# Kernel tuning notes

Measured on AMD Instinct MI355X. Metric: run time of the kernel, lower is better.

The kernel has to match this reference:

```python
import jax, jax.numpy as jnp
import numpy as np

LN_EPS = 1e-5
SCALE = 1.0 / 8.0  # 1/sqrt(dim/num_heads) = 1/sqrt(64)


def layernorm(x, g, b):
    m = jnp.mean(x, axis=-1, keepdims=True)
    v = jnp.mean(jnp.square(x - m), axis=-1, keepdims=True)
    return (x - m) * jax.lax.rsqrt(v + LN_EPS) * g + b


def attention_block(q_in, kv_in, wq, bq, wk, bk, wv, bv, g, b):
    # un-split single-matrix attention, faithful to the source (no head reshape)
    Q = q_in @ wq + bq            # [B,S,D]
    K = kv_in @ wk + bk           # [B,T,D]
    V = kv_in @ wv + bv           # [B,T,D]
    scores = jnp.einsum('bsd,btd->bst', Q, K) * SCALE  # [B,S,T]
    A = jax.nn.softmax(scores, axis=-1)
    out = jnp.einsum('bst,btd->bsd', A, V)
    return layernorm(out + q_in, g, b)


def setup_inputs() -> dict:
    key = jax.random.key(0)
    ks = jax.random.split(key, 16)
    B, S, T, D = 4, 2048, 2048, 1024
    w = lambda k: jax.random.normal(k, (D, D), dtype=jnp.float32) * 0.02
    z = jnp.zeros((D,), dtype=jnp.float32)
    o = jnp.ones((D,), dtype=jnp.float32)
    return {
        'x': jax.random.normal(ks[0], (B, S, D), dtype=jnp.float32),
        'y': jax.random.normal(ks[1], (B, T, D), dtype=jnp.float32),
        'wq_m': w(ks[2]), 'bq_m': z, 'wk_m': w(ks[3]), 'bk_m': z,
        'wv_m': w(ks[4]), 'bv_m': z, 'g_m': o, 'b_m': z,
        'wq_c': w(ks[5]), 'bq_c': z, 'wk_c': w(ks[6]), 'bk_c': z,
        'wv_c': w(ks[7]), 'bv_c': z, 'g_c': o, 'b_c': z,
        'f0_w': w(ks[8]), 'f0_b': z, 'f1_w': w(ks[9]), 'f1_b': z,
        'g_d': o, 'b_d': z,
    }


def reference(x, y,
              wq_m, bq_m, wk_m, bk_m, wv_m, bv_m, g_m, b_m,
              wq_c, bq_c, wk_c, bk_c, wv_c, bv_c, g_c, b_c,
              f0_w, f0_b, f1_w, f1_b, g_d, b_d):
    # masked (self) attention + shared decoder LN residual
    res = x
    x = layernorm(attention_block(x, x, wq_m, bq_m, wk_m, bk_m, wv_m, bv_m, g_m, b_m) + res, g_d, b_d)
    # cross attention against memory y
    res = x
    x = layernorm(attention_block(x, y, wq_c, bq_c, wk_c, bk_c, wv_c, bv_c, g_c, b_c) + res, g_d, b_d)
    # FFN: loop condition in source is always true -> GELU (exact) after every layer
    res = x
    x = jax.nn.gelu(x @ f0_w + f0_b, approximate=False)
    x = jax.nn.gelu(x @ f1_w + f1_b, approximate=False)
    return layernorm(x + res, g_d, b_d)
```

## Files before the change

kernel.cpp:

```cpp
#include <hip/hip_runtime.h>

#define DEV __device__ __forceinline__

typedef __attribute__((ext_vector_type(8))) short bf16x8;
typedef __attribute__((ext_vector_type(4))) float f32x4;

DEV float bf2f(unsigned short u) { return __uint_as_float(((unsigned int)u) << 16); }
DEV unsigned short f2bf(float f) {
    unsigned int x = __float_as_uint(f);
    return (unsigned short)((x + 0x7fffu + ((x >> 16) & 1u)) >> 16);
}
DEV float gelu_exact(float x) { return 0.5f * x * (1.0f + erff(x * 0.7071067811865475f)); }

DEV void gload16(const void* g, void* l) {
    __builtin_amdgcn_global_load_lds((const __attribute__((address_space(1))) void*)g,
                                     (__attribute__((address_space(3))) void*)l, 16, 0, 0);
}

template <int OFF>
DEV bf16x8 ds_read128(unsigned addr) {
    bf16x8 r;
    asm volatile("ds_read_b128 %0, %1 offset:%2" : "=v"(r) : "v"(addr), "i"(OFF));
    return r;
}

__global__ __launch_bounds__(256) void transpose_cast_w(const float* __restrict__ in,
                                                        unsigned short* __restrict__ out,
                                                        int R, int C) {
    __shared__ float tile[32][33];
    int c0 = blockIdx.x * 32, r0 = blockIdx.y * 32;
    int tx = threadIdx.x, ty = threadIdx.y;
#pragma unroll
    for (int i = 0; i < 32; i += 8)
        tile[ty + i][tx] = in[(size_t)(r0 + ty + i) * C + (c0 + tx)];
    __syncthreads();
#pragma unroll
    for (int i = 0; i < 32; i += 8)
        out[(size_t)(c0 + ty + i) * R + (r0 + tx)] = f2bf(tile[tx][ty + i]);
}

__global__ __launch_bounds__(256) void cast_f32_bf16(const float* __restrict__ in,
                                                     unsigned short* __restrict__ out, int n4) {
    int i = blockIdx.x * 256 + threadIdx.x;
    if (i >= n4) return;
    float4 v = ((const float4*)in)[i];
    unsigned short o[4] = {f2bf(v.x), f2bf(v.y), f2bf(v.z), f2bf(v.w)};
    *(uint2*)(out + (size_t)i * 4) = *(uint2*)o;
}


template <int H>
DEV void mfma16q(const bf16x8 (&a)[2][2], const bf16x8 (&b)[4][2], f32x4 (&acc)[4][4]) {
#pragma unroll
    for (int ks = 0; ks < 2; ++ks)
#pragma unroll
        for (int n = 0; n < 4; ++n) {
            acc[2 * H][n]     = __builtin_amdgcn_mfma_f32_16x16x32_bf16(a[0][ks], b[n][ks], acc[2 * H][n], 0, 0, 0);
            acc[2 * H + 1][n] = __builtin_amdgcn_mfma_f32_16x16x32_bf16(a[1][ks], b[n][ks], acc[2 * H + 1][n], 0, 0, 0);
        }
}

template <int BIAS_MODE, bool GELU_ACT, bool OUT_F32>
__global__ __launch_bounds__(256, 2) void gemm128(const unsigned short* __restrict__ A,
                                                  const unsigned short* __restrict__ BT,
                                                  const float* __restrict__ bias,
                                                  float* __restrict__ Cf,
                                                  unsigned short* __restrict__ Cb,
                                                  int N, int K, int lda, int ldb, float scale,
                                                  long sA, long sB, long sC, long sBias) {
    const int gx = gridDim.x, gy = gridDim.y;
    int f = blockIdx.x + gx * (blockIdx.y + gy * blockIdx.z);
    const int nwg = gx * gy * gridDim.z;
    f = (f & 7) * (nwg >> 3) + (f >> 3);
    const int bz = f / (gx * gy);
    const int rem = f - bz * gx * gy;
    const int by = rem / gx;
    const int bx = rem - by * gx;

    A += (long)bz * sA;
    BT += (long)bz * sB;
    if (BIAS_MODE) bias += (long)bz * sBias;

    const int tid = threadIdx.x;
    const int lane = tid & 63;
    const int wave = tid >> 6;
    const int wr = wave >> 1;
    const int wc = wave & 1;
    const int llo = lane & 15, lhi = lane >> 4;
    const int bm = bx * 128, bn = by * 128;

    __shared__ unsigned short lds[2][2][128 * 64];

    const int xk0 = (0 + lhi) ^ (llo & 7);
    const int xk1 = (4 + lhi) ^ (llo & 7);

    const unsigned base0 = (unsigned)(size_t)&lds[0][0][0];
    const unsigned aA0 = base0 + (unsigned)(wr * 64 + llo) * 128u + xk0 * 16;
    const unsigned aA1 = base0 + (unsigned)(wr * 64 + llo) * 128u + xk1 * 16;
    const unsigned aB0 = base0 + (unsigned)(wc * 64 + llo) * 128u + xk0 * 16;
    const unsigned aB1 = base0 + (unsigned)(wc * 64 + llo) * 128u + xk1 * 16;

    int srow[4], sq[4];
#pragma unroll
    for (int L = 0; L < 4; ++L) {
        const int d = L * 256 + tid;
        srow[L] = d >> 3;
        sq[L] = (d & 7) ^ (srow[L] & 7);
    }
    const unsigned short* gA = A + (size_t)bm * lda;
    const unsigned short* gB = BT + (size_t)bn * ldb;

#define SA(kt, BUF)                                                                     \
    {                                                                                   \
        _Pragma("unroll") for (int L = 0; L < 4; ++L)                                   \
            gload16(gA + (size_t)srow[L] * lda + (kt) + sq[L] * 8,                      \
                    &lds[BUF][0][(L * 256 + wave * 64) * 8]);                           \
    }
#define SB(kt, BUF)                                                                     \
    {                                                                                   \
        _Pragma("unroll") for (int L = 0; L < 4; ++L)                                   \
            gload16(gB + (size_t)srow[L] * ldb + (kt) + sq[L] * 8,                      \
                    &lds[BUF][1][(L * 256 + wave * 64) * 8]);                           \
    }

    f32x4 acc[4][4] = {};
    bf16x8 b[4][2];

#define PH(H, BUF, LOADB, STG, TAIL)                                         \
    {                                                                        \
        STG;                                                                 \
        bf16x8 afr[2][2];                                                    \
        afr[0][0] = ds_read128<(BUF)*32768 + (H)*4096 + 0>(aA0);             \
        afr[0][1] = ds_read128<(BUF)*32768 + (H)*4096 + 0>(aA1);             \
        afr[1][0] = ds_read128<(BUF)*32768 + (H)*4096 + 2048>(aA0);          \
        afr[1][1] = ds_read128<(BUF)*32768 + (H)*4096 + 2048>(aA1);          \
        if (LOADB) {                                                         \
            b[0][0] = ds_read128<(BUF)*32768 + 16384 + 0>(aB0);              \
            b[0][1] = ds_read128<(BUF)*32768 + 16384 + 0>(aB1);              \
            b[1][0] = ds_read128<(BUF)*32768 + 16384 + 2048>(aB0);           \
            b[1][1] = ds_read128<(BUF)*32768 + 16384 + 2048>(aB1);           \
            b[2][0] = ds_read128<(BUF)*32768 + 16384 + 4096>(aB0);           \
            b[2][1] = ds_read128<(BUF)*32768 + 16384 + 4096>(aB1);           \
            b[3][0] = ds_read128<(BUF)*32768 + 16384 + 6144>(aB0);           \
            b[3][1] = ds_read128<(BUF)*32768 + 16384 + 6144>(aB1);           \
        }                                                                    \
        __builtin_amdgcn_s_barrier();                                        \
        asm volatile("s_waitcnt lgkmcnt(0)" :::);                            \
        __builtin_amdgcn_sched_barrier(0);                                   \
        __builtin_amdgcn_s_setprio(1);                                       \
        mfma16q<H>(afr, b, acc);                                             \
        __builtin_amdgcn_s_setprio(0);                                       \
        TAIL;                                                                \
        __builtin_amdgcn_s_barrier();                                        \
    }

#define VM0 asm volatile("s_waitcnt vmcnt(0)" :::)
#define NOP ((void)0)

    const int nt = K >> 6;

    SA(0, 0);
    SB(0, 0);
    VM0;
    __builtin_amdgcn_s_barrier();

    int kt = 0;
    for (int t = 0; t < nt; t += 2) {
        const bool st0 = (t + 1 < nt);
        const bool st1 = (t + 2 < nt);
        PH(0, 0, true,  if (st0) { SA(kt + 64, 1); SB(kt + 64, 1); }, NOP);
        PH(1, 0, false, NOP, VM0);
        PH(0, 1, true,  if (st1) { SA(kt + 128, 0); SB(kt + 128, 0); }, NOP);
        PH(1, 1, false, NOP, VM0);
        kt += 128;
    }
#undef PH
#undef SA
#undef SB
#undef VM0
#undef NOP

#pragma unroll
    for (int m = 0; m < 4; ++m) {
#pragma unroll
        for (int n = 0; n < 4; ++n) {
            const int col = bn + wc * 64 + n * 16 + llo;
            float bcol = 0.f;
            if constexpr (BIAS_MODE == 1) bcol = bias[col];
#pragma unroll
            for (int j = 0; j < 4; ++j) {
                const int row = bm + wr * 64 + m * 16 + lhi * 4 + j;
                float v = acc[m][n][j] * scale + bcol;
                if constexpr (BIAS_MODE == 2) v += bias[row];
                if constexpr (GELU_ACT) v = gelu_exact(v);
                const size_t idx = (size_t)bz * (size_t)sC + (size_t)row * N + col;
                if constexpr (OUT_F32) Cf[idx] = v;
                else Cb[idx] = f2bf(v);
            }
        }
    }
}

__global__ __launch_bounds__(256) void softmax_rows(unsigned short* __restrict__ s, int T) {
    __shared__ float red[4];
    unsigned short* p = s + (size_t)blockIdx.x * T;
    const int tid = threadIdx.x;

    uint4 raw = *(const uint4*)(p + tid * 8);
    const unsigned short* u = (const unsigned short*)&raw;
    float v[8];
#pragma unroll
    for (int j = 0; j < 8; ++j) v[j] = bf2f(u[j]);

    float mx = -3.4e38f;
#pragma unroll
    for (int j = 0; j < 8; ++j) mx = fmaxf(mx, v[j]);
#pragma unroll
    for (int o = 32; o; o >>= 1) mx = fmaxf(mx, __shfl_xor(mx, o));
    if ((tid & 63) == 0) red[tid >> 6] = mx;
    __syncthreads();
    mx = fmaxf(fmaxf(red[0], red[1]), fmaxf(red[2], red[3]));
    __syncthreads();

    float sum = 0.f;
#pragma unroll
    for (int j = 0; j < 8; ++j) {
        v[j] = expf(v[j] - mx);
        sum += v[j];
    }
#pragma unroll
    for (int o = 32; o; o >>= 1) sum += __shfl_xor(sum, o);
    if ((tid & 63) == 0) red[tid >> 6] = sum;
    __syncthreads();
    sum = red[0] + red[1] + red[2] + red[3];
    const float inv = 1.0f / sum;

    unsigned short o8[8];
#pragma unroll
    for (int j = 0; j < 8; ++j) o8[j] = f2bf(v[j] * inv);
    *(uint4*)(p + tid * 8) = *(uint4*)o8;
}

DEV float block_sum(float v, float* red, int tid) {
#pragma unroll
    for (int o = 32; o; o >>= 1) v += __shfl_xor(v, o);
    if ((tid & 63) == 0) red[tid >> 6] = v;
    __syncthreads();
    v = red[0] + red[1] + red[2] + red[3];
    __syncthreads();
    return v;
}

__global__ __launch_bounds__(256) void ln_double(const float* __restrict__ av,
                                                 const float* __restrict__ xin,
                                                 const float* __restrict__ g1, const float* __restrict__ b1,
                                                 const float* __restrict__ g2, const float* __restrict__ b2,
                                                 float* __restrict__ xout,
                                                 unsigned short* __restrict__ xbf, int D) {
    __shared__ float red[4];
    const int tid = threadIdx.x;
    const size_t base = (size_t)blockIdx.x * D + tid * 4;
    const float4 a4 = *(const float4*)(av + base);
    const float4 x4 = *(const float4*)(xin + base);
    float x[4] = {x4.x, x4.y, x4.z, x4.w};
    float t[4] = {a4.x + x[0], a4.y + x[1], a4.z + x[2], a4.w + x[3]};
    const float invD = 1.0f / D;

    float m = block_sum(t[0] + t[1] + t[2] + t[3], red, tid) * invD;
    float q = 0.f;
#pragma unroll
    for (int j = 0; j < 4; ++j) q += (t[j] - m) * (t[j] - m);
    q = block_sum(q, red, tid) * invD;
    float rs = rsqrtf(q + 1e-5f);

    float u[4];
#pragma unroll
    for (int j = 0; j < 4; ++j) {
        const int idx = tid * 4 + j;
        u[j] = (t[j] - m) * rs * g1[idx] + b1[idx] + x[j];
    }
    float m2 = block_sum(u[0] + u[1] + u[2] + u[3], red, tid) * invD;
    float q2 = 0.f;
#pragma unroll
    for (int j = 0; j < 4; ++j) q2 += (u[j] - m2) * (u[j] - m2);
    q2 = block_sum(q2, red, tid) * invD;
    float rs2 = rsqrtf(q2 + 1e-5f);

    float4 o4;
    unsigned short ob[4];
#pragma unroll
    for (int j = 0; j < 4; ++j) {
        const int idx = tid * 4 + j;
        float o = (u[j] - m2) * rs2 * g2[idx] + b2[idx];
        ((float*)&o4)[j] = o;
        ob[j] = f2bf(o);
    }
    *(float4*)(xout + base) = o4;
    *(uint2*)(xbf + base) = *(uint2*)ob;
}

__global__ __launch_bounds__(256) void ln_single(const float* __restrict__ a,
                                                 const float* __restrict__ b_,
                                                 const float* __restrict__ g, const float* __restrict__ bb,
                                                 float* __restrict__ out, int D) {
    __shared__ float red[4];
    const int tid = threadIdx.x;
    const size_t base = (size_t)blockIdx.x * D + tid * 4;
    const float4 a4 = *(const float4*)(a + base);
    const float4 x4 = *(const float4*)(b_ + base);
    float t[4] = {a4.x + x4.x, a4.y + x4.y, a4.z + x4.z, a4.w + x4.w};
    const float invD = 1.0f / D;
    float m = block_sum(t[0] + t[1] + t[2] + t[3], red, tid) * invD;
    float q = 0.f;
#pragma unroll
    for (int j = 0; j < 4; ++j) q += (t[j] - m) * (t[j] - m);
    q = block_sum(q, red, tid) * invD;
    float rs = rsqrtf(q + 1e-5f);
    float4 o4;
#pragma unroll
    for (int j = 0; j < 4; ++j) {
        const int idx = tid * 4 + j;
        ((float*)&o4)[j] = (t[j] - m) * rs * g[idx] + bb[idx];
    }
    *(float4*)(out + base) = o4;
}

extern "C" void kernel_launch(void* const* d_in, const int* in_sizes, int n_in,
                              void* d_out, int out_size, void* d_ws, size_t ws_size,
                              hipStream_t stream) {
    (void)in_sizes; (void)n_in; (void)out_size; (void)ws_size;
    constexpr int B = 4, S = 2048, T = 2048, D = 1024;
    constexpr int M = B * S;
    constexpr long MD = (long)M * D;
    constexpr long ST = (long)S * T;
    constexpr long DD = (long)D * D;

    const float* x = (const float*)d_in[0];
    const float* y = (const float*)d_in[1];
    const float* w_in[8] = {(const float*)d_in[2],  (const float*)d_in[4],  (const float*)d_in[6],
                            (const float*)d_in[10], (const float*)d_in[12], (const float*)d_in[14],
                            (const float*)d_in[18], (const float*)d_in[20]};
    const float* bq_m = (const float*)d_in[3];
    const float* bk_m = (const float*)d_in[5];
    const float* bv_m = (const float*)d_in[7];
    const float* g_m = (const float*)d_in[8];
    const float* b_m = (const float*)d_in[9];
    const float* bq_c = (const float*)d_in[11];
    const float* bk_c = (const float*)d_in[13];
    const float* bv_c = (const float*)d_in[15];
    const float* g_c = (const float*)d_in[16];
    const float* b_c = (const float*)d_in[17];
    const float* f0_b = (const float*)d_in[19];
    const float* f1_b = (const float*)d_in[21];
    const float* g_d = (const float*)d_in[22];
    const float* b_d = (const float*)d_in[23];
    float* dout = (float*)d_out;

    char* p = (char*)d_ws;
    auto carve = [&](size_t bytes) { void* r = p; p += (bytes + 255) & ~(size_t)255; return r; };
    float* xcur = (float*)carve(MD * 4);
    unsigned short* wT = (unsigned short*)carve((size_t)8 * DD * 2);
    unsigned short* abf = (unsigned short*)carve(MD * 2);
    unsigned short* ybf = (unsigned short*)carve(MD * 2);
    unsigned short* Qb = (unsigned short*)carve(MD * 2);
    unsigned short* Kb = (unsigned short*)carve(MD * 2);
    unsigned short* Vt = (unsigned short*)carve(MD * 2);
    unsigned short* scores = (unsigned short*)carve((size_t)B * ST * 2);
    float* tmp = (float*)carve(MD * 4);
    float* bqk_m = (float*)carve(2 * D * 4);
    float* bqk_c = (float*)carve(2 * D * 4);

    const dim3 blk256(256);
    const dim3 tb(32, 8);

    for (int w = 0; w < 8; ++w)
        transpose_cast_w<<<dim3(32, 32), tb, 0, stream>>>(w_in[w], wT + (size_t)w * DD, D, D);
    cast_f32_bf16<<<dim3(M * D / 4 / 256), blk256, 0, stream>>>(x, abf, M * D / 4);
    cast_f32_bf16<<<dim3(M * D / 4 / 256), blk256, 0, stream>>>(y, ybf, M * D / 4);
    hipMemcpyAsync(bqk_m, bq_m, D * 4, hipMemcpyDeviceToDevice, stream);
    hipMemcpyAsync(bqk_m + D, bk_m, D * 4, hipMemcpyDeviceToDevice, stream);
    hipMemcpyAsync(bqk_c, bq_c, D * 4, hipMemcpyDeviceToDevice, stream);
    hipMemcpyAsync(bqk_c + D, bk_c, D * 4, hipMemcpyDeviceToDevice, stream);

    unsigned short* wqm = wT + 0 * DD;
    unsigned short* wvm = wT + 2 * DD;
    unsigned short* wqc = wT + 3 * DD;
    unsigned short* wvc = wT + 5 * DD;
    unsigned short* wf0 = wT + 6 * DD;
    unsigned short* wf1 = wT + 7 * DD;

    const dim3 gQK(M / 128, D / 128, 2);
    const dim3 gVt(D / 128, T / 128, B);
    const dim3 gScores(S / 128, T / 128, B);
    const dim3 gPV(S / 128, D / 128, B);
    const dim3 gFFN(M / 128, D / 128, 1);

    gemm128<1, false, false><<<gQK, blk256, 0, stream>>>(abf, wqm, bqk_m, nullptr, Qb, D, D, D, D, 1.f, 0, DD, MD, D);
    gemm128<2, false, false><<<gVt, blk256, 0, stream>>>(wvm, abf, bv_m, nullptr, Vt, T, D, D, D, 1.f, 0, (long)S * D, (long)D * T, 0);
    gemm128<0, false, false><<<gScores, blk256, 0, stream>>>(Qb, Kb, nullptr, nullptr, scores, T, D, D, D, 0.125f, (long)S * D, (long)T * D, ST, 0);
    softmax_rows<<<dim3(B * S), blk256, 0, stream>>>(scores, T);
    gemm128<0, false, true><<<gPV, blk256, 0, stream>>>(scores, Vt, nullptr, tmp, nullptr, D, T, T, T, 1.f, ST, (long)T * D, (long)S * D, 0);
    ln_double<<<dim3(M), blk256, 0, stream>>>(tmp, x, g_m, b_m, g_d, b_d, xcur, abf, D);

    gemm128<1, false, false><<<gQK, blk256, 0, stream>>>(abf, wqc, bqk_c, nullptr, Qb, D, D, D, D, 1.f, MD, DD, MD, D);
    gemm128<2, false, false><<<gVt, blk256, 0, stream>>>(wvc, ybf, bv_c, nullptr, Vt, T, D, D, D, 1.f, 0, (long)S * D, (long)D * T, 0);
    gemm128<0, false, false><<<gScores, blk256, 0, stream>>>(Qb, Kb, nullptr, nullptr, scores, T, D, D, D, 0.125f, (long)S * D, (long)T * D, ST, 0);
    softmax_rows<<<dim3(B * S), blk256, 0, stream>>>(scores, T);
    gemm128<0, false, true><<<gPV, blk256, 0, stream>>>(scores, Vt, nullptr, tmp, nullptr, D, T, T, T, 1.f, ST, (long)T * D, (long)S * D, 0);
    ln_double<<<dim3(M), blk256, 0, stream>>>(tmp, xcur, g_c, b_c, g_d, b_d, xcur, abf, D);

    gemm128<1, true, false><<<gFFN, blk256, 0, stream>>>(abf, wf0, f0_b, nullptr, Qb, D, D, D, D, 1.f, 0, 0, 0, 0);
    gemm128<1, true, true><<<gFFN, blk256, 0, stream>>>(Qb, wf1, f1_b, tmp, nullptr, D, D, D, D, 1.f, 0, 0, 0, 0);
    ln_single<<<dim3(M), blk256, 0, stream>>>(tmp, xcur, g_d, b_d, dout, D);
}
```

Before: 496.6 us.

## Restructure GEMM mainloop into triple-buffered K=32 tiles with one barrier per tile

The bf16 GEMM mainloop now stages K=32 slices into a three-stage LDS ring (48KB) instead of double-buffered K=64 tiles, issuing prefetches two tiles ahead with vmcnt(4) waits and a single barrier per tile. The LDS swizzle is changed for 64-byte rows, and launch bounds go from 2 to 3 workgroups per CU. The aim is to keep more loads in flight and raise occupancy so global latency is better hidden. The cost is twice as many loop iterations with less MFMA work per barrier, plus tighter register limits.

Result: slower. 523.5 us (+5.4%).

```diff
diff --git a/kernel.cpp b/kernel.cpp
--- a/kernel.cpp
+++ b/kernel.cpp
@@ -49,19 +49,8 @@
 }
 
 
-template <int H>
-DEV void mfma16q(const bf16x8 (&a)[2][2], const bf16x8 (&b)[4][2], f32x4 (&acc)[4][4]) {
-#pragma unroll
-    for (int ks = 0; ks < 2; ++ks)
-#pragma unroll
-        for (int n = 0; n < 4; ++n) {
-            acc[2 * H][n]     = __builtin_amdgcn_mfma_f32_16x16x32_bf16(a[0][ks], b[n][ks], acc[2 * H][n], 0, 0, 0);
-            acc[2 * H + 1][n] = __builtin_amdgcn_mfma_f32_16x16x32_bf16(a[1][ks], b[n][ks], acc[2 * H + 1][n], 0, 0, 0);
-        }
-}
-
 template <int BIAS_MODE, bool GELU_ACT, bool OUT_F32>
-__global__ __launch_bounds__(256, 2) void gemm128(const unsigned short* __restrict__ A,
+__global__ __launch_bounds__(256, 3) void gemm128(const unsigned short* __restrict__ A,
                                                   const unsigned short* __restrict__ BT,
                                                   const float* __restrict__ bias,
                                                   float* __restrict__ Cf,
@@ -89,96 +78,96 @@
     const int llo = lane & 15, lhi = lane >> 4;
     const int bm = bx * 128, bn = by * 128;
 
-    __shared__ unsigned short lds[2][2][128 * 64];
-
-    const int xk0 = (0 + lhi) ^ (llo & 7);
-    const int xk1 = (4 + lhi) ^ (llo & 7);
-
-    const unsigned base0 = (unsigned)(size_t)&lds[0][0][0];
-    const unsigned aA0 = base0 + (unsigned)(wr * 64 + llo) * 128u + xk0 * 16;
-    const unsigned aA1 = base0 + (unsigned)(wr * 64 + llo) * 128u + xk1 * 16;
-    const unsigned aB0 = base0 + (unsigned)(wc * 64 + llo) * 128u + xk0 * 16;
-    const unsigned aB1 = base0 + (unsigned)(wc * 64 + llo) * 128u + xk1 * 16;
-
-    int srow[4], sq[4];
-#pragma unroll
-    for (int L = 0; L < 4; ++L) {
+    __shared__ unsigned char ldsraw[49152];
+    char* ldsc = (char*)&ldsraw[0];
+
+    const unsigned swz = (unsigned)((lhi ^ ((llo >> 1) & 3)) * 16);
+    const unsigned base0 = (unsigned)(size_t)&ldsraw[0];
+    const unsigned aA = base0 + (unsigned)(wr * 64 + llo) * 64u + swz;
+    const unsigned aB = base0 + 8192u + (unsigned)(wc * 64 + llo) * 64u + swz;
+
+    const unsigned short* pA[2];
+    const unsigned short* pB[2];
+#pragma unroll
+    for (int L = 0; L < 2; ++L) {
         const int d = L * 256 + tid;
-        srow[L] = d >> 3;
-        sq[L] = (d & 7) ^ (srow[L] & 7);
-    }
-    const unsigned short* gA = A + (size_t)bm * lda;
-    const unsigned short* gB = BT + (size_t)bn * ldb;
-
-#define SA(kt, BUF)                                                                     \
-    {                                                                                   \
-        _Pragma("unroll") for (int L = 0; L < 4; ++L)                                   \
-            gload16(gA + (size_t)srow[L] * lda + (kt) + sq[L] * 8,                      \
-                    &lds[BUF][0][(L * 256 + wave * 64) * 8]);                           \
-    }
-#define SB(kt, BUF)                                                                     \
-    {                                                                                   \
-        _Pragma("unroll") for (int L = 0; L < 4; ++L)                                   \
-            gload16(gB + (size_t)srow[L] * ldb + (kt) + sq[L] * 8,                      \
-                    &lds[BUF][1][(L * 256 + wave * 64) * 8]);                           \
+        const int r = d >> 2;
+        const int sc = ((d & 3) ^ ((r >> 1) & 3)) * 8;
+        pA[L] = A + (size_t)(bm + r) * lda + sc;
+        pB[L] = BT + (size_t)(bn + r) * ldb + sc;
+    }
+    const unsigned stW = (unsigned)wave * 1024u;
+
+#define STG(ktv, off)                                                        \
+    {                                                                        \
+        gload16(pA[0] + (ktv), ldsc + (off) + 0 * 4096 + stW);               \
+        gload16(pA[1] + (ktv), ldsc + (off) + 1 * 4096 + stW);               \
+        gload16(pB[0] + (ktv), ldsc + (off) + 8192 + 0 * 4096 + stW);        \
+        gload16(pB[1] + (ktv), ldsc + (off) + 8192 + 1 * 4096 + stW);        \
     }
 
     f32x4 acc[4][4] = {};
-    bf16x8 b[4][2];
-
-#define PH(H, BUF, LOADB, STG, TAIL)                                         \
+
+#define VM4 asm volatile("s_waitcnt vmcnt(4)" :::)
+#define VM0 asm volatile("s_waitcnt vmcnt(0)" :::)
+
+#define TILE(WAIT, DO_STAGE, ktv)                                            \
     {                                                                        \
-        STG;                                                                 \
-        bf16x8 afr[2][2];                                                    \
-        afr[0][0] = ds_read128<(BUF)*32768 + (H)*4096 + 0>(aA0);             \
-        afr[0][1] = ds_read128<(BUF)*32768 + (H)*4096 + 0>(aA1);             \
-        afr[1][0] = ds_read128<(BUF)*32768 + (H)*4096 + 2048>(aA0);          \
-        afr[1][1] = ds_read128<(BUF)*32768 + (H)*4096 + 2048>(aA1);          \
-        if (LOADB) {                                                         \
-            b[0][0] = ds_read128<(BUF)*32768 + 16384 + 0>(aB0);              \
-            b[0][1] = ds_read128<(BUF)*32768 + 16384 + 0>(aB1);              \
-            b[1][0] = ds_read128<(BUF)*32768 + 16384 + 2048>(aB0);           \
-            b[1][1] = ds_read128<(BUF)*32768 + 16384 + 2048>(aB1);           \
-            b[2][0] = ds_read128<(BUF)*32768 + 16384 + 4096>(aB0);           \
-            b[2][1] = ds_read128<(BUF)*32768 + 16384 + 4096>(aB1);           \
-            b[3][0] = ds_read128<(BUF)*32768 + 16384 + 6144>(aB0);           \
-            b[3][1] = ds_read128<(BUF)*32768 + 16384 + 6144>(aB1);           \
-        }                                                                    \
+        WAIT;                                                                \
+        __builtin_amdgcn_sched_barrier(0);                                   \
         __builtin_amdgcn_s_barrier();                                        \
+        __builtin_amdgcn_sched_barrier(0);                                   \
+        if (DO_STAGE) STG(ktv, off_s);                                       \
+        const unsigned ar = aA + off_r, br = aB + off_r;                     \
+        bf16x8 a0 = ds_read128<0>(ar);                                       \
+        bf16x8 a1 = ds_read128<1024>(ar);                                    \
+        bf16x8 a2 = ds_read128<2048>(ar);                                    \
+        bf16x8 a3 = ds_read128<3072>(ar);                                    \
+        bf16x8 b0 = ds_read128<0>(br);                                       \
+        bf16x8 b1 = ds_read128<1024>(br);                                    \
+        bf16x8 b2 = ds_read128<2048>(br);                                    \
+        bf16x8 b3 = ds_read128<3072>(br);                                    \
         asm volatile("s_waitcnt lgkmcnt(0)" :::);                            \
         __builtin_amdgcn_sched_barrier(0);                                   \
         __builtin_amdgcn_s_setprio(1);                                       \
-        mfma16q<H>(afr, b, acc);                                             \
+        acc[0][0] = __builtin_amdgcn_mfma_f32_16x16x32_bf16(a0, b0, acc[0][0], 0, 0, 0); \
+        acc[0][1] = __builtin_amdgcn_mfma_f32_16x16x32_bf16(a0, b1, acc[0][1], 0, 0, 0); \
+        acc[0][2] = __builtin_amdgcn_mfma_f32_16x16x32_bf16(a0, b2, acc[0][2], 0, 0, 0); \
+        acc[0][3] = __builtin_amdgcn_mfma_f32_16x16x32_bf16(a0, b3, acc[0][3], 0, 0, 0); \
+        acc[1][0] = __builtin_amdgcn_mfma_f32_16x16x32_bf16(a1, b0, acc[1][0], 0, 0, 0); \
+        acc[1][1] = __builtin_amdgcn_mfma_f32_16x16x32_bf16(a1, b1, acc[1][1], 0, 0, 0); \
+        acc[1][2] = __builtin_amdgcn_mfma_f32_16x16x32_bf16(a1, b2, acc[1][2], 0, 0, 0); \
+        acc[1][3] = __builtin_amdgcn_mfma_f32_16x16x32_bf16(a1, b3, acc[1][3], 0, 0, 0); \
+        acc[2][0] = __builtin_amdgcn_mfma_f32_16x16x32_bf16(a2, b0, acc[2][0], 0, 0, 0); \
+        acc[2][1] = __builtin_amdgcn_mfma_f32_16x16x32_bf16(a2, b1, acc[2][1], 0, 0, 0); \
+        acc[2][2] = __builtin_amdgcn_mfma_f32_16x16x32_bf16(a2, b2, acc[2][2], 0, 0, 0); \
+        acc[2][3] = __builtin_amdgcn_mfma_f32_16x16x32_bf16(a2, b3, acc[2][3], 0, 0, 0); \
+        acc[3][0] = __builtin_amdgcn_mfma_f32_16x16x32_bf16(a3, b0, acc[3][0], 0, 0, 0); \
+        acc[3][1] = __builtin_amdgcn_mfma_f32_16x16x32_bf16(a3, b1, acc[3][1], 0, 0, 0); \
+        acc[3][2] = __builtin_amdgcn_mfma_f32_16x16x32_bf16(a3, b2, acc[3][2], 0, 0, 0); \
+        acc[3][3] = __builtin_amdgcn_mfma_f32_16x16x32_bf16(a3, b3, acc[3][3], 0, 0, 0); \
         __builtin_amdgcn_s_setprio(0);                                       \
-        TAIL;                                                                \
-        __builtin_amdgcn_s_barrier();                                        \
-    }
-
-#define VM0 asm volatile("s_waitcnt vmcnt(0)" :::)
-#define NOP ((void)0)
-
-    const int nt = K >> 6;
-
-    SA(0, 0);
-    SB(0, 0);
-    VM0;
-    __builtin_amdgcn_s_barrier();
-
-    int kt = 0;
-    for (int t = 0; t < nt; t += 2) {
-        const bool st0 = (t + 1 < nt);
-        const bool st1 = (t + 2 < nt);
-        PH(0, 0, true,  if (st0) { SA(kt + 64, 1); SB(kt + 64, 1); }, NOP);
-        PH(1, 0, false, NOP, VM0);
-        PH(0, 1, true,  if (st1) { SA(kt + 128, 0); SB(kt + 128, 0); }, NOP);
-        PH(1, 1, false, NOP, VM0);
-        kt += 128;
-    }
-#undef PH
-#undef SA
-#undef SB
+        off_r = (off_r == 32768u) ? 0u : off_r + 16384u;                     \
+        off_s = (off_s == 32768u) ? 0u : off_s + 16384u;                     \
+    }
+
+    const int nt = K >> 5;
+
+    unsigned off_r = 0u, off_s = 32768u;
+    STG(0, 0u);
+    STG(32, 16384u);
+
+    int ktv = 64;
+    for (int t = 0; t < nt - 2; ++t) {
+        TILE(VM4, true, ktv);
+        ktv += 32;
+    }
+    TILE(VM4, false, 0);
+    TILE(VM0, false, 0);
+#undef TILE
+#undef STG
+#undef VM4
 #undef VM0
-#undef NOP
 
 #pragma unroll
     for (int m = 0; m < 4; ++m) {
```
